# Performance work log

Measured on AMD Instinct MI355X. Metric: run time of the kernel, lower is better.

## Reference

```python
import jax, jax.numpy as jnp
import numpy as np

D = 64          # node_hidden_dim
MP_STEPS = 6    # num_step_message_passing
S2S_STEPS = 6   # num_step_set2set
LSTM_LAYERS = 3 # num_layer_set2set


def setup_inputs() -> dict:
    key = jax.random.key(0)
    ks = jax.random.split(key, 32)
    N, E, B = 10000, 50000, 500
    node_in, edge_in, edge_hid, out_dim = 15, 5, 128, 12
    s = 0.1
    inp = {}
    inp["node_feat"] = jax.random.normal(ks[0], (N, node_in), jnp.float32)
    inp["edge_feat"] = jax.random.normal(ks[1], (E, edge_in), jnp.float32)
    inp["src"] = jax.random.randint(ks[2], (E,), 0, N)
    inp["dst"] = jax.random.randint(ks[3], (E,), 0, N)
    inp["graph_ids"] = jnp.sort(jax.random.randint(ks[4], (N,), 0, B))
    inp["num_graphs"] = B
    # lin0
    inp["lin0_W"] = jax.random.normal(ks[5], (node_in, D), jnp.float32) * s
    inp["lin0_b"] = jnp.zeros((D,), jnp.float32)
    # edge network MLP (Linear -> ReLU -> Linear), output reshaped to D x D per edge
    inp["em_W1"] = jax.random.normal(ks[6], (edge_in, edge_hid), jnp.float32) * s
    inp["em_b1"] = jnp.zeros((edge_hid,), jnp.float32)
    inp["em_W2"] = jax.random.normal(ks[7], (edge_hid, D * D), jnp.float32) * 0.02
    inp["em_b2"] = jnp.zeros((D * D,), jnp.float32)
    inp["conv_bias"] = jnp.zeros((D,), jnp.float32)
    # GRU (input D, hidden D), torch layout: [3*D, in], gate order r,z,n
    inp["gru_Wih"] = jax.random.normal(ks[8], (3 * D, D), jnp.float32) * s
    inp["gru_Whh"] = jax.random.normal(ks[9], (3 * D, D), jnp.float32) * s
    inp["gru_bih"] = jnp.zeros((3 * D,), jnp.float32)
    inp["gru_bhh"] = jnp.zeros((3 * D,), jnp.float32)
    # Set2Set LSTM: input 2*D, hidden D, 3 layers. torch layout [4*D, in], gates i,f,g,o
    inp["lstm0_Wih"] = jax.random.normal(ks[10], (4 * D, 2 * D), jnp.float32) * s
    inp["lstm0_Whh"] = jax.random.normal(ks[11], (4 * D, D), jnp.float32) * s
    inp["lstm0_bih"] = jnp.zeros((4 * D,), jnp.float32)
    inp["lstm0_bhh"] = jnp.zeros((4 * D,), jnp.float32)
    inp["lstm12_Wih"] = jax.random.normal(ks[12], (2, 4 * D, D), jnp.float32) * s
    inp["lstm12_Whh"] = jax.random.normal(ks[13], (2, 4 * D, D), jnp.float32) * s
    inp["lstm12_bih"] = jnp.zeros((2, 4 * D), jnp.float32)
    inp["lstm12_bhh"] = jnp.zeros((2, 4 * D), jnp.float32)
    # output head
    inp["lin1_W"] = jax.random.normal(ks[14], (2 * D, D), jnp.float32) * s
    inp["lin1_b"] = jnp.zeros((D,), jnp.float32)
    inp["lin2_W"] = jax.random.normal(ks[15], (D, out_dim), jnp.float32) * s
    inp["lin2_b"] = jnp.zeros((out_dim,), jnp.float32)
    return inp


def _mpnn(node_feat, edge_feat, src, dst, graph_ids, num_graphs,
          lin0_W, lin0_b, em_W1, em_b1, em_W2, em_b2, conv_bias,
          gru_Wih, gru_Whh, gru_bih, gru_bhh,
          lstm0_Wih, lstm0_Whh, lstm0_bih, lstm0_bhh,
          lstm12_Wih, lstm12_Whh, lstm12_bih, lstm12_bhh,
          lin1_W, lin1_b, lin2_W, lin2_b):
    N = node_feat.shape[0]
    E = edge_feat.shape[0]
    B = num_graphs
    # initial node embedding
    out = jax.nn.relu(node_feat @ lin0_W + lin0_b)      # [N, D]
    h = out                                             # GRU hidden (seq_len=1, 1 layer)
    # per-edge weight matrices (edge features are static across steps)
    We = (jax.nn.relu(edge_feat @ em_W1 + em_b1) @ em_W2 + em_b2).reshape(E, D, D)
    for _ in range(MP_STEPS):
        # NNConv: gather src -> per-edge matvec -> scatter-add to dst
        msg = jnp.einsum('ei,eio->eo', out[src], We)    # [E, D]
        agg = jax.ops.segment_sum(msg, dst, num_segments=N) + conv_bias
        m = jax.nn.relu(agg)                            # [N, D]
        # GRU cell (torch gate order r, z, n)
        gx = m @ gru_Wih.T + gru_bih
        gh = h @ gru_Whh.T + gru_bhh
        rx, zx, nx = jnp.split(gx, 3, axis=-1)
        rh, zh, nh = jnp.split(gh, 3, axis=-1)
        r = jax.nn.sigmoid(rx + rh)
        z = jax.nn.sigmoid(zx + zh)
        n = jnp.tanh(nx + r * nh)
        h = (1.0 - z) * n + z * h
        out = h
    # Set2Set readout: 3-layer LSTM over steps, attention over nodes per graph
    h_l = [jnp.zeros((B, D), out.dtype) for _ in range(LSTM_LAYERS)]
    c_l = [jnp.zeros((B, D), out.dtype) for _ in range(LSTM_LAYERS)]
    q_star = jnp.zeros((B, 2 * D), out.dtype)
    for _ in range(S2S_STEPS):
        x = q_star
        for l in range(LSTM_LAYERS):
            if l == 0:
                Wih, Whh, bih, bhh = lstm0_Wih, lstm0_Whh, lstm0_bih, lstm0_bhh
            else:
                Wih, Whh = lstm12_Wih[l - 1], lstm12_Whh[l - 1]
                bih, bhh = lstm12_bih[l - 1], lstm12_bhh[l - 1]
            g = x @ Wih.T + bih + h_l[l] @ Whh.T + bhh
            i_g, f_g, g_g, o_g = jnp.split(g, 4, axis=-1)
            c_l[l] = jax.nn.sigmoid(f_g) * c_l[l] + jax.nn.sigmoid(i_g) * jnp.tanh(g_g)
            h_l[l] = jax.nn.sigmoid(o_g) * jnp.tanh(c_l[l])
            x = h_l[l]
        q = x                                           # [B, D]
        # segment softmax attention
        e = jnp.sum(out * q[graph_ids], axis=-1)        # [N]
        emax = jax.ops.segment_max(e, graph_ids, num_segments=B)
        ex = jnp.exp(e - emax[graph_ids])
        denom = jax.ops.segment_sum(ex, graph_ids, num_segments=B)
        alpha = ex / denom[graph_ids]                   # [N]
        readout = jax.ops.segment_sum(alpha[:, None] * out, graph_ids, num_segments=B)
        q_star = jnp.concatenate([q, readout], axis=-1) # [B, 2D]
    y = jax.nn.relu(q_star @ lin1_W + lin1_b) @ lin2_W + lin2_b
    return y


def reference(node_feat, edge_feat, src, dst, graph_ids, num_graphs,
              lin0_W, lin0_b, em_W1, em_b1, em_W2, em_b2, conv_bias,
              gru_Wih, gru_Whh, gru_bih, gru_bhh,
              lstm0_Wih, lstm0_Whh, lstm0_bih, lstm0_bhh,
              lstm12_Wih, lstm12_Whh, lstm12_bih, lstm12_bhh,
              lin1_W, lin1_b, lin2_W, lin2_b):
    return _mpnn(node_feat, edge_feat, src, dst, graph_ids, num_graphs,
                 lin0_W, lin0_b, em_W1, em_b1, em_W2, em_b2, conv_bias,
                 gru_Wih, gru_Whh, gru_bih, gru_bhh,
                 lstm0_Wih, lstm0_Whh, lstm0_bih, lstm0_bhh,
                 lstm12_Wih, lstm12_Whh, lstm12_bih, lstm12_bhh,
                 lin1_W, lin1_b, lin2_W, lin2_b)
```

## Files before the change

kernel.cpp:

```cpp
#include <hip/hip_runtime.h>
#include <math.h>

#define NGRAPH 500
#define MP_STEPS 6
#define S2S_STEPS 6
#define S2S_CAP 128

typedef _Float16 h8 __attribute__((ext_vector_type(8)));
typedef float f4 __attribute__((ext_vector_type(4)));

__device__ __forceinline__ float sigmoidf_(float v){ return 1.0f/(1.0f + expf(-v)); }

__global__ void k_zero(float* __restrict__ p, int n){
  int i = blockIdx.x*256 + threadIdx.x;
  if(i < n) p[i] = 0.f;
}

__global__ void k_lin0(const float* __restrict__ nf, const float* __restrict__ W,
                       const float* __restrict__ b, float* __restrict__ x, int N){
  int n = blockIdx.x*4 + (threadIdx.x >> 6);
  int d = threadIdx.x & 63;
  if(n >= N) return;
  float acc = b[d];
#pragma unroll
  for(int i=0;i<15;i++) acc = fmaf(nf[n*15+i], W[i*64+d], acc);
  x[n*64+d] = fmaxf(acc, 0.0f);
}

__global__ void k_edgeh(const float* __restrict__ ef, const float* __restrict__ W1,
                        const float* __restrict__ b1, _Float16* __restrict__ he, int E){
  int e = blockIdx.x;
  int h = threadIdx.x;
  if(e >= E || h >= 160) return;
  float v;
  if(h < 128){
    float acc = b1[h];
#pragma unroll
    for(int i=0;i<5;i++) acc = fmaf(ef[e*5+i], W1[i*128+h], acc);
    v = fmaxf(acc, 0.f);
  } else {
    v = (h == 128) ? 1.0f : 0.0f;
  }
  he[(size_t)e*160 + h] = (_Float16)v;
}

__global__ void k_prepW2(const float* __restrict__ W2, const float* __restrict__ b2,
                         _Float16* __restrict__ W2T){
  int idx = blockIdx.x*256 + threadIdx.x;
  if(idx >= 4096*160) return;
  int n = idx / 160, k = idx % 160;
  float v = (k < 128) ? W2[(size_t)k*4096 + n] : ((k == 128) ? b2[n] : 0.f);
  W2T[idx] = (_Float16)v;
}

__global__ __launch_bounds__(256, 2) void k_fmsg(
    const _Float16* __restrict__ he,
    const _Float16* __restrict__ W2T,
    const float* __restrict__ x,
    const int* __restrict__ src, const int* __restrict__ dst,
    float* __restrict__ agg, int E)
{
  __shared__ _Float16 hs[64*160];
  __shared__ float xsT[64*68];
  __shared__ int ds_dst[64];
  const int tid  = threadIdx.x;
  const int wave = tid >> 6;
  const int lane = tid & 63;
  const int quad = lane >> 4;
  const int l15  = lane & 15;
  const int e0   = blockIdx.x * 64;

  for(int t = tid; t < 1280; t += 256){
    int r = t / 20, c = t % 20;
    uint4 v = make_uint4(0,0,0,0);
    if(e0 + r < E) v = *(const uint4*)&he[(size_t)(e0+r)*160 + c*8];
    *(uint4*)&hs[r*160 + c*8] = v;
  }
  {
    int j = tid >> 2, qc = tid & 3;
    int sj = (e0 + j < E) ? src[e0 + j] : 0;
    const float4* xr = (const float4*)(x + (size_t)sj*64);
#pragma unroll
    for(int k=0;k<4;k++){
      float4 v = xr[qc*4 + k];
      int ib = qc*16 + k*4;
      xsT[(ib+0)*68 + j] = v.x;
      xsT[(ib+1)*68 + j] = v.y;
      xsT[(ib+2)*68 + j] = v.z;
      xsT[(ib+3)*68 + j] = v.w;
    }
  }
  if(tid < 64) ds_dst[tid] = (e0 + tid < E) ? dst[e0 + tid] : 0;
  __syncthreads();

  h8 af[4][5];
#pragma unroll
  for(int mt=0;mt<4;mt++)
#pragma unroll
    for(int ks=0;ks<5;ks++)
      af[mt][ks] = *(const h8*)&hs[(mt*16 + l15)*160 + ks*32 + (quad<<3)];

  const _Float16* bbase = W2T + ((size_t)(wave*16 + l15))*160 + (quad<<3);
  h8 bf[5], bn[5];
#pragma unroll
  for(int ks=0;ks<5;ks++) bf[ks] = *(const h8*)(bbase + ks*32);

  f4 macc[4];
#pragma unroll
  for(int mt=0;mt<4;mt++) macc[mt] = (f4){0.f,0.f,0.f,0.f};

#pragma unroll 2
  for(int i=0;i<64;i++){
    if(i < 63){
      const _Float16* nb = bbase + (size_t)(i+1)*64*160;
#pragma unroll
      for(int ks=0;ks<5;ks++) bn[ks] = *(const h8*)(nb + ks*32);
    }
    f4 g0 = (f4){0.f,0.f,0.f,0.f}, g1 = g0, g2 = g0, g3 = g0;
#pragma unroll
    for(int ks=0;ks<5;ks++){
      g0 = __builtin_amdgcn_mfma_f32_16x16x32_f16(af[0][ks], bf[ks], g0, 0, 0, 0);
      g1 = __builtin_amdgcn_mfma_f32_16x16x32_f16(af[1][ks], bf[ks], g1, 0, 0, 0);
      g2 = __builtin_amdgcn_mfma_f32_16x16x32_f16(af[2][ks], bf[ks], g2, 0, 0, 0);
      g3 = __builtin_amdgcn_mfma_f32_16x16x32_f16(af[3][ks], bf[ks], g3, 0, 0, 0);
    }
    f4 x0 = *(const f4*)&xsT[i*68 +  0 + (quad<<2)];
    f4 x1 = *(const f4*)&xsT[i*68 + 16 + (quad<<2)];
    f4 x2 = *(const f4*)&xsT[i*68 + 32 + (quad<<2)];
    f4 x3 = *(const f4*)&xsT[i*68 + 48 + (quad<<2)];
    macc[0] += x0 * g0;
    macc[1] += x1 * g1;
    macc[2] += x2 * g2;
    macc[3] += x3 * g3;
#pragma unroll
    for(int ks=0;ks<5;ks++) bf[ks] = bn[ks];
  }

  const int col = wave*16 + l15;
#pragma unroll
  for(int mt=0;mt<4;mt++){
#pragma unroll
    for(int r=0;r<4;r++){
      int edge = mt*16 + (quad<<2) + r;
      if(e0 + edge < E)
        atomicAdd(&agg[(size_t)ds_dst[edge]*64 + col], macc[mt][r]);
    }
  }
}

__global__ __launch_bounds__(256) void k_gru2(
    float* __restrict__ x, float* __restrict__ agg, const float* __restrict__ cb,
    const float* __restrict__ WihT, const float* __restrict__ WhhT,
    const float* __restrict__ bih, const float* __restrict__ bhh, int N)
{
  __shared__ float ms[32*64], hs2[32*64];
  const int tid = threadIdx.x;
  const int n0 = blockIdx.x*32;
  for(int t=tid; t<2048; t+=256){
    int n = n0 + (t>>6), d = t&63;
    float mv=0.f, hv=0.f;
    if(n < N){
      mv = fmaxf(agg[(size_t)n*64+d] + cb[d], 0.f);
      agg[(size_t)n*64+d] = 0.f;
      hv = x[(size_t)n*64+d];
    }
    ms[t]=mv; hs2[t]=hv;
  }
  __syncthreads();
  const int gx = tid & 31, ng = tid >> 5;
  float ar[4][2]={{0}}, az[4][2]={{0}}, anx[4][2]={{0}}, anh[4][2]={{0}};
#pragma unroll 4
  for(int k=0;k<64;k++){
    float wi0=WihT[k*192+gx],     wi1=WihT[k*192+gx+32];
    float wi2=WihT[k*192+gx+64],  wi3=WihT[k*192+gx+96];
    float wi4=WihT[k*192+gx+128], wi5=WihT[k*192+gx+160];
    float wh0=WhhT[k*192+gx],     wh1=WhhT[k*192+gx+32];
    float wh2=WhhT[k*192+gx+64],  wh3=WhhT[k*192+gx+96];
    float wh4=WhhT[k*192+gx+128], wh5=WhhT[k*192+gx+160];
#pragma unroll
    for(int j=0;j<4;j++){
      float mk = ms[(ng*4+j)*64+k], hk = hs2[(ng*4+j)*64+k];
      ar[j][0] = fmaf(mk,wi0, fmaf(hk,wh0, ar[j][0]));
      ar[j][1] = fmaf(mk,wi1, fmaf(hk,wh1, ar[j][1]));
      az[j][0] = fmaf(mk,wi2, fmaf(hk,wh2, az[j][0]));
      az[j][1] = fmaf(mk,wi3, fmaf(hk,wh3, az[j][1]));
      anx[j][0]= fmaf(mk,wi4, anx[j][0]);
      anx[j][1]= fmaf(mk,wi5, anx[j][1]);
      anh[j][0]= fmaf(hk,wh4, anh[j][0]);
      anh[j][1]= fmaf(hk,wh5, anh[j][1]);
    }
  }
#pragma unroll
  for(int j=0;j<4;j++){
    int n = n0 + ng*4 + j;
    if(n >= N) continue;
#pragma unroll
    for(int c=0;c<2;c++){
      int d = gx + 32*c;
      float r  = sigmoidf_(ar[j][c] + bih[d]     + bhh[d]);
      float z  = sigmoidf_(az[j][c] + bih[64+d]  + bhh[64+d]);
      float nn = tanhf(anx[j][c] + bih[128+d] + r*(anh[j][c] + bhh[128+d]));
      float hv = hs2[(ng*4+j)*64+d];
      x[(size_t)n*64+d] = (1.f - z)*nn + z*hv;
    }
  }
}

__global__ void k_tr_gru(const float* __restrict__ Wih, const float* __restrict__ Whh,
                         float* __restrict__ WihT, float* __restrict__ WhhT){
  int idx = blockIdx.x*256 + threadIdx.x;
  if(idx < 192*64){
    int r = idx/64, i = idx%64;
    WihT[i*192 + r] = Wih[idx];
    WhhT[i*192 + r] = Whh[idx];
  }
}

__global__ void k_tr_lstm(const float* __restrict__ w0ih, const float* __restrict__ w0hh,
                          const float* __restrict__ w12ih, const float* __restrict__ w12hh,
                          float* __restrict__ t0ih, float* __restrict__ t0hh,
                          float* __restrict__ t12ih, float* __restrict__ t12hh){
  int idx = blockIdx.x*256 + threadIdx.x;
  if(idx < 256*128){ int r = idx/128, k = idx%128; t0ih[k*256+r] = w0ih[idx]; }
  if(idx < 256*64){ int r = idx/64, k = idx%64; t0hh[k*256+r] = w0hh[idx]; }
  if(idx < 2*256*64){
    int l = idx/(256*64); int rem = idx%(256*64); int r = rem/64, k = rem%64;
    t12ih[l*64*256 + k*256 + r] = w12ih[idx];
    t12hh[l*64*256 + k*256 + r] = w12hh[idx];
  }
}

__device__ __forceinline__ int lbound(const int* __restrict__ a, int n, int v){
  int lo=0, hi=n;
  while(lo<hi){ int mid=(lo+hi)>>1; if(a[mid]<v) lo=mid+1; else hi=mid; }
  return lo;
}

template<int IN>
__device__ __forceinline__ void lstm_layer(
    const float* __restrict__ xin, float* __restrict__ hv, float* __restrict__ cv,
    const float* __restrict__ WihT, const float* __restrict__ WhhT,
    const float* __restrict__ bi, const float* __restrict__ bh,
    float* __restrict__ gs, int t)
{
  float a0=0.f,a1=0.f,a2=0.f,a3=0.f;
#pragma unroll
  for(int k=0;k<IN;k+=4){
    a0 = fmaf(xin[k+0], WihT[(k+0)*256+t], a0);
    a1 = fmaf(xin[k+1], WihT[(k+1)*256+t], a1);
    a2 = fmaf(xin[k+2], WihT[(k+2)*256+t], a2);
    a3 = fmaf(xin[k+3], WihT[(k+3)*256+t], a3);
  }
#pragma unroll
  for(int k=0;k<64;k+=4){
    a0 = fmaf(hv[k+0], WhhT[(k+0)*256+t], a0);
    a1 = fmaf(hv[k+1], WhhT[(k+1)*256+t], a1);
    a2 = fmaf(hv[k+2], WhhT[(k+2)*256+t], a2);
    a3 = fmaf(hv[k+3], WhhT[(k+3)*256+t], a3);
  }
  gs[t] = (a0+a1)+(a2+a3) + bi[t] + bh[t];
  __syncthreads();
  if(t < 64){
    float ig = sigmoidf_(gs[t]);
    float fg = sigmoidf_(gs[64+t]);
    float gg = tanhf(gs[128+t]);
    float og = sigmoidf_(gs[192+t]);
    float cn = fg*cv[t] + ig*gg;
    cv[t] = cn;
    hv[t] = og*tanhf(cn);
  }
  __syncthreads();
}

__global__ __launch_bounds__(256) void k_s2s(
    const float* __restrict__ x, const int* __restrict__ gid, int N,
    const float* __restrict__ t0ih, const float* __restrict__ t0hh,
    const float* __restrict__ l0_bih, const float* __restrict__ l0_bhh,
    const float* __restrict__ t12ih, const float* __restrict__ t12hh,
    const float* __restrict__ l12_bih, const float* __restrict__ l12_bhh,
    const float* __restrict__ W1, const float* __restrict__ b1,
    const float* __restrict__ W2, const float* __restrict__ b2,
    float* __restrict__ y)
{
  const int b = blockIdx.x;
  const int t = threadIdx.x;
  const int wave = t >> 6, lane = t & 63;
  __shared__ float xt[S2S_CAP*64];
  __shared__ float hsl[3][64], csl[3][64], qs[128], gs[256];
  __shared__ float ps[S2S_CAP], rop[4*64], wred[4], wsum[4];
  __shared__ int sh_n0, sh_n1;

  if(t == 0) sh_n0 = lbound(gid, N, b);
  if(t == 1) sh_n1 = lbound(gid, N, b+1);
  if(t < 192){ hsl[t>>6][t&63] = 0.f; csl[t>>6][t&63] = 0.f; }
  if(t < 128) qs[t] = 0.f;
  __syncthreads();
  const int n0 = sh_n0, cnt = sh_n1 - sh_n0;
  const int cc = (cnt < S2S_CAP) ? cnt : S2S_CAP;

  for(int j = wave; j < cc; j += 4)
    xt[j*64 + lane] = x[(size_t)(n0+j)*64 + lane];
  __syncthreads();

  for(int step=0; step<S2S_STEPS; step++){
    lstm_layer<128>(qs,     hsl[0], csl[0], t0ih,           t0hh,           l0_bih,        l0_bhh,        gs, t);
    lstm_layer<64>(hsl[0],  hsl[1], csl[1], t12ih,          t12hh,          l12_bih,       l12_bhh,       gs, t);
    lstm_layer<64>(hsl[1],  hsl[2], csl[2], t12ih + 64*256, t12hh + 64*256, l12_bih + 256, l12_bhh + 256, gs, t);

    float qv = hsl[2][lane];
    float pm = -1e30f;
    for(int j = wave; j < cc; j += 4){
      float p = xt[j*64 + lane] * qv;
#pragma unroll
      for(int o=32;o;o>>=1) p += __shfl_xor(p, o, 64);
      if(lane == 0) ps[j] = p;
      pm = fmaxf(pm, p);
    }
    for(int j = S2S_CAP + wave; j < cnt; j += 4){
      float p = x[(size_t)(n0+j)*64 + lane] * qv;
#pragma unroll
      for(int o=32;o;o>>=1) p += __shfl_xor(p, o, 64);
      pm = fmaxf(pm, p);
    }
    if(lane == 0) wred[wave] = pm;
    __syncthreads();
    float mx = fmaxf(fmaxf(wred[0],wred[1]), fmaxf(wred[2],wred[3]));

    float pro = 0.f, pssum = 0.f;
    for(int j = wave; j < cc; j += 4){
      float ex = expf(ps[j] - mx);
      pssum += ex;
      pro = fmaf(ex, xt[j*64 + lane], pro);
    }
    for(int j = S2S_CAP + wave; j < cnt; j += 4){
      float xv = x[(size_t)(n0+j)*64 + lane];
      float p = xv * qv;
#pragma unroll
      for(int o=32;o;o>>=1) p += __shfl_xor(p, o, 64);
      float ex = expf(p - mx);
      pssum += ex;
      pro = fmaf(ex, xv, pro);
    }
    rop[wave*64 + lane] = pro;
    if(lane == 0) wsum[wave] = pssum;
    __syncthreads();
    if(t < 64){
      float tot = wsum[0]+wsum[1]+wsum[2]+wsum[3];
      float inv = (tot > 0.f) ? 1.f/tot : 0.f;
      float rv = (rop[t] + rop[64+t] + rop[128+t] + rop[192+t]) * inv;
      qs[t] = hsl[2][t];
      qs[64+t] = rv;
    }
    __syncthreads();
  }
  if(t < 64){
    float a = b1[t];
#pragma unroll 4
    for(int k=0;k<128;k++) a = fmaf(qs[k], W1[k*64+t], a);
    gs[t] = fmaxf(a, 0.f);
  }
  __syncthreads();
  if(t < 12){
    float o = b2[t];
#pragma unroll 4
    for(int k=0;k<64;k++) o = fmaf(gs[k], W2[k*12+t], o);
    y[b*12+t] = o;
  }
}

extern "C" void kernel_launch(void* const* d_in, const int* in_sizes, int n_in,
                              void* d_out, int out_size, void* d_ws, size_t ws_size,
                              hipStream_t stream) {
  const float* node_feat = (const float*)d_in[0];
  const float* edge_feat = (const float*)d_in[1];
  const int*   src       = (const int*)d_in[2];
  const int*   dst       = (const int*)d_in[3];
  const int*   gid       = (const int*)d_in[4];
  const float* lin0_W = (const float*)d_in[6];
  const float* lin0_b = (const float*)d_in[7];
  const float* em_W1  = (const float*)d_in[8];
  const float* em_b1  = (const float*)d_in[9];
  const float* em_W2  = (const float*)d_in[10];
  const float* em_b2  = (const float*)d_in[11];
  const float* conv_b = (const float*)d_in[12];
  const float* gru_Wih = (const float*)d_in[13];
  const float* gru_Whh = (const float*)d_in[14];
  const float* gru_bih = (const float*)d_in[15];
  const float* gru_bhh = (const float*)d_in[16];
  const float* l0_Wih = (const float*)d_in[17];
  const float* l0_Whh = (const float*)d_in[18];
  const float* l0_bih = (const float*)d_in[19];
  const float* l0_bhh = (const float*)d_in[20];
  const float* l12_Wih = (const float*)d_in[21];
  const float* l12_Whh = (const float*)d_in[22];
  const float* l12_bih = (const float*)d_in[23];
  const float* l12_bhh = (const float*)d_in[24];
  const float* lin1_W = (const float*)d_in[25];
  const float* lin1_b = (const float*)d_in[26];
  const float* lin2_W = (const float*)d_in[27];
  const float* lin2_b = (const float*)d_in[28];
  float* y = (float*)d_out;

  const int N = in_sizes[0] / 15;
  const int E = in_sizes[1] / 5;
  const int B = NGRAPH;

  char* p = (char*)d_ws;
  auto carve = [&](size_t bytes)->char* {
    char* r = p; p += (bytes + 255) & ~(size_t)255; return r;
  };
  _Float16* he_h = (_Float16*)carve((size_t)E*160*2);
  _Float16* W2T  = (_Float16*)carve((size_t)4096*160*2);
  float* x     = (float*)carve((size_t)N*64*4);
  float* agg   = (float*)carve((size_t)N*64*4);
  float* gWihT = (float*)carve(192*64*4);
  float* gWhhT = (float*)carve(192*64*4);
  float* t0ih  = (float*)carve(128*256*4);
  float* t0hh  = (float*)carve(64*256*4);
  float* t12ih = (float*)carve(2*64*256*4);
  float* t12hh = (float*)carve(2*64*256*4);
  (void)ws_size; (void)n_in; (void)out_size;

  k_lin0<<<(N+3)/4, 256, 0, stream>>>(node_feat, lin0_W, lin0_b, x, N);
  k_edgeh<<<E, 192, 0, stream>>>(edge_feat, em_W1, em_b1, he_h, E);
  k_prepW2<<<(4096*160+255)/256, 256, 0, stream>>>(em_W2, em_b2, W2T);
  k_tr_gru<<<(192*64+255)/256, 256, 0, stream>>>(gru_Wih, gru_Whh, gWihT, gWhhT);
  k_tr_lstm<<<(2*256*64+255)/256, 256, 0, stream>>>(l0_Wih, l0_Whh, l12_Wih, l12_Whh,
                                                    t0ih, t0hh, t12ih, t12hh);
  k_zero<<<(N*64+255)/256, 256, 0, stream>>>(agg, N*64);

  const int nblk = (E + 63) / 64;
  for(int s=0; s<MP_STEPS; s++){
    k_fmsg<<<nblk, 256, 0, stream>>>(he_h, W2T, x, src, dst, agg, E);
    k_gru2<<<(N+31)/32, 256, 0, stream>>>(x, agg, conv_b, gWihT, gWhhT, gru_bih, gru_bhh, N);
  }

  k_s2s<<<B, 256, 0, stream>>>(x, gid, N,
                               t0ih, t0hh, l0_bih, l0_bhh,
                               t12ih, t12hh, l12_bih, l12_bhh,
                               lin1_W, lin1_b, lin2_W, lin2_b, y);
}
```

Before: 951.6 us.

## Restructure Set2Set LSTM with concatenated weights, split-K float4 matvec, per-thread attention dots

Concatenates each LSTM layer's input and hidden weights into one [K,256] matrix. Each wave now handles a quarter of K and reads float4 weight vectors, and the partial sums are reduced in shared memory. Bias sums are precomputed once per block. Attention scores are now computed one node per thread from a padded shared tile (stride 65) in place of a wave shuffle reduction per node, which cuts shuffle and sync overhead in the Set2Set kernel. The trade-off is an extra shared-memory reduction pass and more shared memory per block.

```diff
diff --git a/kernel.cpp b/kernel.cpp
--- a/kernel.cpp
+++ b/kernel.cpp
@@ -216,17 +216,20 @@
   }
 }
 
-__global__ void k_tr_lstm(const float* __restrict__ w0ih, const float* __restrict__ w0hh,
-                          const float* __restrict__ w12ih, const float* __restrict__ w12hh,
-                          float* __restrict__ t0ih, float* __restrict__ t0hh,
-                          float* __restrict__ t12ih, float* __restrict__ t12hh){
+__global__ void k_tr_lstmcat(const float* __restrict__ w0ih, const float* __restrict__ w0hh,
+                             const float* __restrict__ w12ih, const float* __restrict__ w12hh,
+                             float* __restrict__ W0cat, float* __restrict__ W12cat){
   int idx = blockIdx.x*256 + threadIdx.x;
-  if(idx < 256*128){ int r = idx/128, k = idx%128; t0ih[k*256+r] = w0ih[idx]; }
-  if(idx < 256*64){ int r = idx/64, k = idx%64; t0hh[k*256+r] = w0hh[idx]; }
-  if(idx < 2*256*64){
-    int l = idx/(256*64); int rem = idx%(256*64); int r = rem/64, k = rem%64;
-    t12ih[l*64*256 + k*256 + r] = w12ih[idx];
-    t12hh[l*64*256 + k*256 + r] = w12hh[idx];
+  if(idx < 192*256){
+    int k = idx / 256, r = idx % 256;
+    W0cat[idx] = (k < 128) ? w0ih[r*128 + k] : w0hh[r*64 + (k - 128)];
+  }
+  if(idx < 2*128*256){
+    int l = idx / (128*256);
+    int rem = idx % (128*256);
+    int k = rem / 256, r = rem % 256;
+    W12cat[idx] = (k < 64) ? w12ih[((size_t)l*256 + r)*64 + k]
+                           : w12hh[((size_t)l*256 + r)*64 + (k - 64)];
   }
 }
 
@@ -236,35 +239,39 @@
   return lo;
 }
 
-template<int IN>
-__device__ __forceinline__ void lstm_layer(
+template<int KTOT>
+__device__ __forceinline__ void lstm_layer2(
     const float* __restrict__ xin, float* __restrict__ hv, float* __restrict__ cv,
-    const float* __restrict__ WihT, const float* __restrict__ WhhT,
-    const float* __restrict__ bi, const float* __restrict__ bh,
-    float* __restrict__ gs, int t)
+    const float* __restrict__ Wcat, const float* __restrict__ bsum,
+    f4* __restrict__ ps4, int t)
 {
-  float a0=0.f,a1=0.f,a2=0.f,a3=0.f;
-#pragma unroll
-  for(int k=0;k<IN;k+=4){
-    a0 = fmaf(xin[k+0], WihT[(k+0)*256+t], a0);
-    a1 = fmaf(xin[k+1], WihT[(k+1)*256+t], a1);
-    a2 = fmaf(xin[k+2], WihT[(k+2)*256+t], a2);
-    a3 = fmaf(xin[k+3], WihT[(k+3)*256+t], a3);
-  }
-#pragma unroll
-  for(int k=0;k<64;k+=4){
-    a0 = fmaf(hv[k+0], WhhT[(k+0)*256+t], a0);
-    a1 = fmaf(hv[k+1], WhhT[(k+1)*256+t], a1);
-    a2 = fmaf(hv[k+2], WhhT[(k+2)*256+t], a2);
-    a3 = fmaf(hv[k+3], WhhT[(k+3)*256+t], a3);
-  }
-  gs[t] = (a0+a1)+(a2+a3) + bi[t] + bh[t];
+  constexpr int CH = KTOT/4;
+  const int kc = t >> 6, tq = t & 63;
+  const float* wp = Wcat + (size_t)(kc*CH)*256 + 4*tq;
+  const float* xp = xin + kc*CH;
+  f4 acc = (f4){0.f,0.f,0.f,0.f};
+#pragma unroll
+  for(int i=0;i<CH;i++){
+    f4 w = *(const f4*)(wp + (size_t)i*256);
+    acc += xp[i] * w;
+  }
+  ps4[t] = acc;
   __syncthreads();
   if(t < 64){
-    float ig = sigmoidf_(gs[t]);
-    float fg = sigmoidf_(gs[64+t]);
-    float gg = tanhf(gs[128+t]);
-    float og = sigmoidf_(gs[192+t]);
+    float v[4];
+#pragma unroll
+    for(int g=0; g<4; g++){
+      int G = g*64 + t;
+      int q = G >> 2, cmp = G & 3;
+      float s = 0.f;
+#pragma unroll
+      for(int k2=0; k2<4; k2++) s += ps4[k2*64 + q][cmp];
+      v[g] = s + bsum[G];
+    }
+    float ig = sigmoidf_(v[0]);
+    float fg = sigmoidf_(v[1]);
+    float gg = tanhf(v[2]);
+    float og = sigmoidf_(v[3]);
     float cn = fg*cv[t] + ig*gg;
     cv[t] = cn;
     hv[t] = og*tanhf(cn);
@@ -274,9 +281,8 @@
 
 __global__ __launch_bounds__(256) void k_s2s(
     const float* __restrict__ x, const int* __restrict__ gid, int N,
-    const float* __restrict__ t0ih, const float* __restrict__ t0hh,
+    const float* __restrict__ W0cat, const float* __restrict__ W12cat,
     const float* __restrict__ l0_bih, const float* __restrict__ l0_bhh,
-    const float* __restrict__ t12ih, const float* __restrict__ t12hh,
     const float* __restrict__ l12_bih, const float* __restrict__ l12_bhh,
     const float* __restrict__ W1, const float* __restrict__ b1,
     const float* __restrict__ W2, const float* __restrict__ b2,
@@ -285,85 +291,103 @@
   const int b = blockIdx.x;
   const int t = threadIdx.x;
   const int wave = t >> 6, lane = t & 63;
-  __shared__ float xt[S2S_CAP*64];
-  __shared__ float hsl[3][64], csl[3][64], qs[128], gs[256];
-  __shared__ float ps[S2S_CAP], rop[4*64], wred[4], wsum[4];
+  __shared__ float xt[S2S_CAP*65];
+  __shared__ float qcat[320];
+  __shared__ float csl[192];
+  __shared__ f4    ps4[256];
+  __shared__ float bsum[768];
+  __shared__ float ps[S2S_CAP];
+  __shared__ float rop[256];
+  __shared__ float wred[4], wsum[4];
   __shared__ int sh_n0, sh_n1;
 
   if(t == 0) sh_n0 = lbound(gid, N, b);
   if(t == 1) sh_n1 = lbound(gid, N, b+1);
-  if(t < 192){ hsl[t>>6][t&63] = 0.f; csl[t>>6][t&63] = 0.f; }
-  if(t < 128) qs[t] = 0.f;
+  for(int i=t; i<320; i+=256) qcat[i] = 0.f;
+  if(t < 192) csl[t] = 0.f;
+  for(int i=t; i<768; i+=256){
+    int layer = i >> 8, g = i & 255;
+    float bi, bh;
+    if(layer == 0){ bi = l0_bih[g]; bh = l0_bhh[g]; }
+    else { bi = l12_bih[(layer-1)*256+g]; bh = l12_bhh[(layer-1)*256+g]; }
+    bsum[i] = bi + bh;
+  }
   __syncthreads();
   const int n0 = sh_n0, cnt = sh_n1 - sh_n0;
   const int cc = (cnt < S2S_CAP) ? cnt : S2S_CAP;
 
   for(int j = wave; j < cc; j += 4)
-    xt[j*64 + lane] = x[(size_t)(n0+j)*64 + lane];
+    xt[j*65 + lane] = x[(size_t)(n0+j)*64 + lane];
   __syncthreads();
 
   for(int step=0; step<S2S_STEPS; step++){
-    lstm_layer<128>(qs,     hsl[0], csl[0], t0ih,           t0hh,           l0_bih,        l0_bhh,        gs, t);
-    lstm_layer<64>(hsl[0],  hsl[1], csl[1], t12ih,          t12hh,          l12_bih,       l12_bhh,       gs, t);
-    lstm_layer<64>(hsl[1],  hsl[2], csl[2], t12ih + 64*256, t12hh + 64*256, l12_bih + 256, l12_bhh + 256, gs, t);
-
-    float qv = hsl[2][lane];
-    float pm = -1e30f;
-    for(int j = wave; j < cc; j += 4){
-      float p = xt[j*64 + lane] * qv;
-#pragma unroll
-      for(int o=32;o;o>>=1) p += __shfl_xor(p, o, 64);
-      if(lane == 0) ps[j] = p;
-      pm = fmaxf(pm, p);
-    }
+    lstm_layer2<192>(qcat,       qcat+128, csl,     W0cat,            bsum,       ps4, t);
+    lstm_layer2<128>(qcat+128,   qcat+192, csl+64,  W12cat,           bsum+256,   ps4, t);
+    lstm_layer2<128>(qcat+192,   qcat+256, csl+128, W12cat+128*256,   bsum+512,   ps4, t);
+
+    const float* q = qcat + 256;
+    float accd = 0.f;
+    if(t < cc){
+      const float* xr = xt + t*65;
+#pragma unroll 8
+      for(int k=0;k<64;k++) accd = fmaf(xr[k], q[k], accd);
+    }
+    float pm = (t < cc) ? accd : -1e30f;
+    float qv = q[lane];
     for(int j = S2S_CAP + wave; j < cnt; j += 4){
       float p = x[(size_t)(n0+j)*64 + lane] * qv;
 #pragma unroll
       for(int o=32;o;o>>=1) p += __shfl_xor(p, o, 64);
       pm = fmaxf(pm, p);
     }
+#pragma unroll
+    for(int o=32;o;o>>=1) pm = fmaxf(pm, __shfl_xor(pm, o, 64));
     if(lane == 0) wred[wave] = pm;
     __syncthreads();
     float mx = fmaxf(fmaxf(wred[0],wred[1]), fmaxf(wred[2],wred[3]));
 
-    float pro = 0.f, pssum = 0.f;
-    for(int j = wave; j < cc; j += 4){
-      float ex = expf(ps[j] - mx);
-      pssum += ex;
-      pro = fmaf(ex, xt[j*64 + lane], pro);
-    }
+    float ex = 0.f;
+    if(t < cc){ ex = expf(accd - mx); ps[t] = ex; }
+    float exsum = ex;
+    float racc = 0.f;
     for(int j = S2S_CAP + wave; j < cnt; j += 4){
       float xv = x[(size_t)(n0+j)*64 + lane];
       float p = xv * qv;
 #pragma unroll
       for(int o=32;o;o>>=1) p += __shfl_xor(p, o, 64);
-      float ex = expf(p - mx);
-      pssum += ex;
-      pro = fmaf(ex, xv, pro);
-    }
-    rop[wave*64 + lane] = pro;
-    if(lane == 0) wsum[wave] = pssum;
+      float e2 = expf(p - mx);
+      if(lane == 0) exsum += e2;
+      racc = fmaf(e2, xv, racc);
+    }
+#pragma unroll
+    for(int o=32;o;o>>=1) exsum += __shfl_xor(exsum, o, 64);
+    if(lane == 0) wsum[wave] = exsum;
+    __syncthreads();
+
+    for(int j = wave; j < cc; j += 4)
+      racc = fmaf(ps[j], xt[j*65 + lane], racc);
+    rop[wave*64 + lane] = racc;
     __syncthreads();
     if(t < 64){
       float tot = wsum[0]+wsum[1]+wsum[2]+wsum[3];
       float inv = (tot > 0.f) ? 1.f/tot : 0.f;
       float rv = (rop[t] + rop[64+t] + rop[128+t] + rop[192+t]) * inv;
-      qs[t] = hsl[2][t];
-      qs[64+t] = rv;
+      qcat[t] = qcat[256+t];
+      qcat[64+t] = rv;
     }
     __syncthreads();
   }
   if(t < 64){
     float a = b1[t];
 #pragma unroll 4
-    for(int k=0;k<128;k++) a = fmaf(qs[k], W1[k*64+t], a);
-    gs[t] = fmaxf(a, 0.f);
+    for(int k=0;k<128;k++) a = fmaf(qcat[k], W1[k*64+t], a);
+    rop[t] = fmaxf(a, 0.f);
   }
   __syncthreads();
   if(t < 12){
     float o = b2[t];
 #pragma unroll 4
-    for(int k=0;k<64;k++) o = fmaf(gs[k], W2[k*12+t], o);
+    for(int k=0;k<64;k++) o = fmaf(rop[k], W2[k*12+t], o);
     y[b*12+t] = o;
   }
 }
@@ -411,22 +435,20 @@
   };
   _Float16* he_h = (_Float16*)carve((size_t)E*160*2);
   _Float16* W2T  = (_Float16*)carve((size_t)4096*160*2);
-  float* x     = (float*)carve((size_t)N*64*4);
-  float* agg   = (float*)carve((size_t)N*64*4);
-  float* gWihT = (float*)carve(192*64*4);
-  float* gWhhT = (float*)carve(192*64*4);
-  float* t0ih  = (float*)carve(128*256*4);
-  float* t0hh  = (float*)carve(64*256*4);
-  float* t12ih = (float*)carve(2*64*256*4);
-  float* t12hh = (float*)carve(2*64*256*4);
+  float* x      = (float*)carve((size_t)N*64*4);
+  float* agg    = (float*)carve((size_t)N*64*4);
+  float* gWihT  = (float*)carve(192*64*4);
+  float* gWhhT  = (float*)carve(192*64*4);
+  float* W0cat  = (float*)carve(192*256*4);
+  float* W12cat = (float*)carve(2*128*256*4);
   (void)ws_size; (void)n_in; (void)out_size;
 
   k_lin0<<<(N+3)/4, 256, 0, stream>>>(node_feat, lin0_W, lin0_b, x, N);
   k_edgeh<<<E, 192, 0, stream>>>(edge_feat, em_W1, em_b1, he_h, E);
   k_prepW2<<<(4096*160+255)/256, 256, 0, stream>>>(em_W2, em_b2, W2T);
   k_tr_gru<<<(192*64+255)/256, 256, 0, stream>>>(gru_Wih, gru_Whh, gWihT, gWhhT);
-  k_tr_lstm<<<(2*256*64+255)/256, 256, 0, stream>>>(l0_Wih, l0_Whh, l12_Wih, l12_Whh,
-                                                    t0ih, t0hh, t12ih, t12hh);
+  k_tr_lstmcat<<<(2*128*256+255)/256, 256, 0, stream>>>(l0_Wih, l0_Whh, l12_Wih, l12_Whh,
+                                                        W0cat, W12cat);
   k_zero<<<(N*64+255)/256, 256, 0, stream>>>(agg, N*64);
 
   const int nblk = (E + 63) / 64;
@@ -436,7 +458,7 @@
   }
 
   k_s2s<<<B, 256, 0, stream>>>(x, gid, N,
-                               t0ih, t0hh, l0_bih, l0_bhh,
-                               t12ih, t12hh, l12_bih, l12_bhh,
+                               W0cat, W12cat, l0_bih, l0_bhh,
+                               l12_bih, l12_bhh,
                                lin1_W, lin1_b, lin2_W, lin2_b, y);
 }
```

New measurement: 908.4 us. 4.5% less time.
